# Kernel optimization log

Measured on AMD Instinct MI355X. Metric: run time of the kernel, lower is better.

The kernel has to match this reference:

```python
import jax, jax.numpy as jnp
import numpy as np

B, S, D = 2, 2048, 1024
H = 16
DK = D // H
SCALE = 1.0 / np.sqrt(DK)

def setup_inputs() -> dict:
    key = jax.random.key(0)
    ks = jax.random.split(key, 11)
    std = 1.0 / np.sqrt(D)
    return {
        "query": jax.random.normal(ks[0], (B, S, D), jnp.float32),
        "key":   jax.random.normal(ks[1], (B, S, D), jnp.float32),
        "value": jax.random.normal(ks[2], (B, S, D), jnp.float32),
        "Wq": jax.random.normal(ks[3], (D, H * DK), jnp.float32) * std,
        "bq": jnp.zeros((H * DK,), jnp.float32),
        "Wk": jax.random.normal(ks[4], (D, H * DK), jnp.float32) * std,
        "bk": jnp.zeros((H * DK,), jnp.float32),
        "Wv": jax.random.normal(ks[5], (D, H * DK), jnp.float32) * std,
        "bv": jnp.zeros((H * DK,), jnp.float32),
        "Wo": jax.random.normal(ks[6], (D, D), jnp.float32) * std,
        "bo": jnp.zeros((D,), jnp.float32),
    }

def reference(query, key, value, Wq, bq, Wk, bk, Wv, bv, Wo, bo):
    b, s, _ = query.shape
    # projections -> [b, s, h, d_k]
    q = (query @ Wq + bq).reshape(b, s, H, DK)
    k = (key   @ Wk + bk).reshape(b, s, H, DK)
    v = (value @ Wv + bv).reshape(b, s, H, DK)
    # scores [b, i, j, h]
    scores = jnp.einsum('bihd,bjhd->bijh', q, k) * SCALE
    attn = jax.nn.softmax(scores, axis=2)  # softmax over key dim j
    # dropout rate 0.0 (eval mode) -> identity
    x = jnp.einsum('bijh,bjhd->bihd', attn, v).reshape(b, s, H * DK)
    return x @ Wo + bo
```

## Files before the change

### kernel.cpp

```cpp
#include <hip/hip_runtime.h>
#include <hip/hip_bf16.h>
#include <math.h>
#include <stdint.h>

constexpr int Bb = 2, Ss = 2048, Dd = 1024, Hh = 16;
constexpr int Mm = Bb * Ss;
constexpr int Nn = Dd;
constexpr int Kk = Dd;
constexpr float QSCALE = 0.125f * 1.44269504088896340736f;

typedef unsigned short ushort_t;
typedef __attribute__((ext_vector_type(8))) short bf16x8;
typedef __attribute__((ext_vector_type(4))) float f32x4;

#if __has_builtin(__builtin_amdgcn_exp2f)
#define EXP2F(x) __builtin_amdgcn_exp2f(x)
#else
#define EXP2F(x) exp2f(x)
#endif

__device__ __forceinline__ ushort_t f2bf(float f) {
  union { float f; unsigned u; } v; v.f = f;
  return (ushort_t)((v.u + 0x7fff + ((v.u >> 16) & 1)) >> 16);
}

__device__ __forceinline__ void load16_lds(const void* g, void* l) {
  __builtin_amdgcn_global_load_lds(
      (const __attribute__((address_space(1))) void*)(uintptr_t)g,
      (__attribute__((address_space(3))) void*)(uint32_t)(uintptr_t)l, 16, 0, 0);
}

__global__ __launch_bounds__(256) void convert_qkv(
    const float* __restrict__ q, const float* __restrict__ k,
    const float* __restrict__ v, ushort_t* __restrict__ out) {
  const int z = blockIdx.z;
  const float* src = (z == 0) ? q : (z == 1) ? k : v;
  ushort_t* dst = out + (size_t)z * Mm * Kk;
  const size_t idx = ((size_t)blockIdx.x * 256 + threadIdx.x) * 4;
  const float4 val = *(const float4*)(src + idx);
  ushort4 o;
  o.x = f2bf(val.x); o.y = f2bf(val.y); o.z = f2bf(val.z); o.w = f2bf(val.w);
  *(ushort4*)(dst + idx) = o;
}

__global__ __launch_bounds__(256) void transpose_w(
    const float* __restrict__ Wq, const float* __restrict__ Wk,
    const float* __restrict__ Wv, const float* __restrict__ Wo,
    ushort_t* __restrict__ Wt) {
  const int z = blockIdx.z;
  const float* W = (z == 0) ? Wq : (z == 1) ? Wk : (z == 2) ? Wv : Wo;
  ushort_t* out = Wt + (size_t)z * Kk * Nn;
  __shared__ float t[64][65];
  const int tid = threadIdx.x;
  const int n0 = blockIdx.x * 64, k0 = blockIdx.y * 64;
  const int lr = tid >> 4, lc = (tid & 15) * 4;
#pragma unroll
  for (int i = 0; i < 4; i++) {
    const int r = lr + i * 16;
    const float4 v = *(const float4*)(W + (size_t)(k0 + r) * Nn + n0 + lc);
    t[r][lc] = v.x; t[r][lc + 1] = v.y; t[r][lc + 2] = v.z; t[r][lc + 3] = v.w;
  }
  __syncthreads();
  const int n = tid >> 2, kc = (tid & 3) * 16;
  ushort_t tmp[16];
#pragma unroll
  for (int j = 0; j < 16; j++) tmp[j] = f2bf(t[kc + j][n]);
  ushort_t* op = out + (size_t)(n0 + n) * Kk + k0 + kc;
  ((uint4*)op)[0] = ((uint4*)tmp)[0];
  ((uint4*)op)[1] = ((uint4*)tmp)[1];
}

template <int BN, bool OUT_BF16>
__global__ __launch_bounds__(256) void gemm_mfma(
    const ushort_t* __restrict__ Abase, size_t a_stride,
    const ushort_t* __restrict__ Wbase, size_t w_stride,
    const float* __restrict__ bias0, const float* __restrict__ bias1,
    const float* __restrict__ bias2, void* __restrict__ Cbase, size_t c_stride,
    float scale_z0, ushort_t* __restrict__ vt_out) {
  constexpr int BM = 128, BK = 32;
  constexpr int WM = (BN == 128) ? 64 : 32;
  constexpr int MT_ = WM / 16, NT_ = 4;
  __shared__ ushort_t As[BM * BK];
  __shared__ ushort_t Bs[BN * BK];
  const int tid = threadIdx.x, lane = tid & 63, wid = tid >> 6;
  const int z = blockIdx.z;
  const ushort_t* A = Abase + (size_t)z * a_stride;
  const ushort_t* Wt = Wbase + (size_t)z * w_stride;
  const float* bias = (z == 0) ? bias0 : (z == 1) ? bias1 : bias2;
  const float sc = (z == 0) ? scale_z0 : 1.0f;
  const int m0 = blockIdx.y * BM, n0 = blockIdx.x * BN;
  const int wm = (BN == 128) ? (wid >> 1) * 64 : wid * 32;
  const int wn = (BN == 128) ? (wid & 1) * 64 : 0;
  const int quad = lane >> 4, r16 = lane & 15;
  const int srow = lane >> 2;
  const int scol = (lane & 3) * 8;

  f32x4 acc[MT_][NT_];
#pragma unroll
  for (int m = 0; m < MT_; m++)
#pragma unroll
    for (int n = 0; n < NT_; n++) acc[m][n] = f32x4{0.f, 0.f, 0.f, 0.f};

  for (int k0 = 0; k0 < Kk; k0 += BK) {
    __syncthreads();
#pragma unroll
    for (int i = 0; i < BM / 64; i++) {
      const int I = wid * (BM / 64) + i;
      load16_lds(A + (size_t)(m0 + I * 16 + srow) * Kk + k0 + scol, As + I * 512);
    }
#pragma unroll
    for (int i = 0; i < BN / 64; i++) {
      const int I = wid * (BN / 64) + i;
      load16_lds(Wt + (size_t)(n0 + I * 16 + srow) * Kk + k0 + scol, Bs + I * 512);
    }
    __syncthreads();
    bf16x8 af[MT_], bfr[NT_];
#pragma unroll
    for (int m = 0; m < MT_; m++)
      af[m] = *(const bf16x8*)(As + (wm + m * 16 + r16) * BK + quad * 8);
#pragma unroll
    for (int n = 0; n < NT_; n++)
      bfr[n] = *(const bf16x8*)(Bs + (wn + n * 16 + r16) * BK + quad * 8);
#pragma unroll
    for (int m = 0; m < MT_; m++)
#pragma unroll
      for (int n = 0; n < NT_; n++)
        acc[m][n] =
            __builtin_amdgcn_mfma_f32_16x16x32_bf16(af[m], bfr[n], acc[m][n], 0, 0, 0);
  }

  if (vt_out != nullptr && z == 2) {
#pragma unroll
    for (int m = 0; m < MT_; m++) {
      const int gr0 = m0 + wm + m * 16 + quad * 4;
      const int bb = gr0 >> 11, s = gr0 & 2047;
#pragma unroll
      for (int n = 0; n < NT_; n++) {
        const int gc = n0 + wn + n * 16 + r16;
        const float bv = bias[gc];
        ushort4 o;
        o.x = f2bf(acc[m][n][0] + bv);
        o.y = f2bf(acc[m][n][1] + bv);
        o.z = f2bf(acc[m][n][2] + bv);
        o.w = f2bf(acc[m][n][3] + bv);
        *(ushort4*)(vt_out + ((size_t)bb * Dd + gc) * Ss + s) = o;
      }
    }
    return;
  }
#pragma unroll
  for (int m = 0; m < MT_; m++) {
#pragma unroll
    for (int n = 0; n < NT_; n++) {
      const int gc = n0 + wn + n * 16 + r16;
      const float bv = bias[gc];
#pragma unroll
      for (int r = 0; r < 4; r++) {
        const int gr = m0 + wm + m * 16 + quad * 4 + r;
        const float v = (acc[m][n][r] + bv) * sc;
        if (OUT_BF16)
          ((ushort_t*)Cbase)[(size_t)z * c_stride + (size_t)gr * Nn + gc] = f2bf(v);
        else
          ((float*)Cbase)[(size_t)z * c_stride + (size_t)gr * Nn + gc] = v;
      }
    }
  }
}

__global__ __launch_bounds__(256) void flash_mfma(
    const ushort_t* __restrict__ Qp, const ushort_t* __restrict__ Kp,
    const ushort_t* __restrict__ Vt, ushort_t* __restrict__ Xp) {
  __shared__ ushort_t Ks[64 * 64];
  __shared__ ushort_t Vts[64 * 64];
  __shared__ ushort_t Ps[64 * 72];
  const int tid = threadIdx.x, lane = tid & 63, wid = tid >> 6;
  const int qt = blockIdx.x, h = blockIdx.y, b = blockIdx.z;
  const int quad = lane >> 4, r16 = lane & 15;
  const int row8 = lane >> 3;
  const int colsw = ((lane & 7) ^ (row8 & 7)) * 8;
  const int swz = (r16 & 7);

  const int qrow = wid * 16 + r16;
  const ushort_t* Qg = Qp + ((size_t)(b * Ss + qt * 64)) * Dd + h * 64;
  const ushort_t* Kg = Kp + ((size_t)b * Ss) * Dd + h * 64;
  const ushort_t* Vg = Vt + ((size_t)b * Dd + h * 64) * Ss;

  bf16x8 qf[2];
#pragma unroll
  for (int ks = 0; ks < 2; ks++)
    qf[ks] = *(const bf16x8*)(Qg + (size_t)qrow * Dd + ks * 32 + quad * 8);

  f32x4 acc[4];
  float rs = 0.f;
#pragma unroll
  for (int mt = 0; mt < 4; mt++) acc[mt] = f32x4{0.f, 0.f, 0.f, 0.f};

  for (int kt = 0; kt < Ss / 64; kt++) {
    __syncthreads();
#pragma unroll
    for (int i = 0; i < 2; i++) {
      const int I = wid * 2 + i;
      load16_lds(Kg + (size_t)(kt * 64 + I * 8 + row8) * Dd + colsw, Ks + I * 512);
      load16_lds(Vg + (size_t)(I * 8 + row8) * Ss + kt * 64 + colsw, Vts + I * 512);
    }
    __syncthreads();

    f32x4 sacc[4];
#pragma unroll
    for (int mm = 0; mm < 4; mm++) sacc[mm] = f32x4{0.f, 0.f, 0.f, 0.f};
#pragma unroll
    for (int ks = 0; ks < 2; ks++) {
      bf16x8 kf[4];
#pragma unroll
      for (int mm = 0; mm < 4; mm++)
        kf[mm] = *(const bf16x8*)(
            Ks + (mm * 16 + r16) * 64 + (((ks * 4 + quad) ^ swz) * 8));
#pragma unroll
      for (int mm = 0; mm < 4; mm++)
        sacc[mm] = __builtin_amdgcn_mfma_f32_16x16x32_bf16(
            kf[mm], qf[ks], sacc[mm], 0, 0, 0);
    }

#pragma unroll
    for (int mm = 0; mm < 4; mm++) {
      float p0 = EXP2F(sacc[mm][0]), p1 = EXP2F(sacc[mm][1]);
      float p2 = EXP2F(sacc[mm][2]), p3 = EXP2F(sacc[mm][3]);
      rs += (p0 + p1) + (p2 + p3);
      union { __hip_bfloat162 h; unsigned u; } lo, hi;
      lo.h = __float22bfloat162_rn(make_float2(p0, p1));
      hi.h = __float22bfloat162_rn(make_float2(p2, p3));
      *(uint2*)(Ps + qrow * 72 + mm * 16 + quad * 4) = make_uint2(lo.u, hi.u);
    }

#pragma unroll
    for (int ks = 0; ks < 2; ks++) {
      bf16x8 vf[4];
#pragma unroll
      for (int mt = 0; mt < 4; mt++)
        vf[mt] = *(const bf16x8*)(
            Vts + (mt * 16 + r16) * 64 + (((ks * 4 + quad) ^ swz) * 8));
      const bf16x8 pf = *(const bf16x8*)(Ps + qrow * 72 + ks * 32 + quad * 8);
#pragma unroll
      for (int mt = 0; mt < 4; mt++)
        acc[mt] = __builtin_amdgcn_mfma_f32_16x16x32_bf16(
            vf[mt], pf, acc[mt], 0, 0, 0);
    }
  }

  rs += __shfl_xor(rs, 16, 64);
  rs += __shfl_xor(rs, 32, 64);
  const float inv = 1.0f / rs;

#pragma unroll
  for (int mt = 0; mt < 4; mt++) {
    ushort4 o;
    o.x = f2bf(acc[mt][0] * inv);
    o.y = f2bf(acc[mt][1] * inv);
    o.z = f2bf(acc[mt][2] * inv);
    o.w = f2bf(acc[mt][3] * inv);
    *(ushort4*)(Xp + (size_t)(b * Ss + qt * 64 + qrow) * Dd +
                h * 64 + mt * 16 + quad * 4) = o;
  }
}

extern "C" void kernel_launch(void* const* d_in, const int* in_sizes, int n_in,
                              void* d_out, int out_size, void* d_ws,
                              size_t ws_size, hipStream_t stream) {
  const float* q  = (const float*)d_in[0];
  const float* k  = (const float*)d_in[1];
  const float* v  = (const float*)d_in[2];
  const float* Wq = (const float*)d_in[3];
  const float* bq = (const float*)d_in[4];
  const float* Wk = (const float*)d_in[5];
  const float* bk = (const float*)d_in[6];
  const float* Wv = (const float*)d_in[7];
  const float* bv = (const float*)d_in[8];
  const float* Wo = (const float*)d_in[9];
  const float* bo = (const float*)d_in[10];

  ushort_t* ws = (ushort_t*)d_ws;
  const size_t MD = (size_t)Mm * Kk;
  const size_t KN = (size_t)Kk * Nn;
  ushort_t* qkvb = ws;
  ushort_t* Wt   = ws + 3 * MD;
  ushort_t* QKVp = Wt + 4 * KN;
  ushort_t* Vtp  = QKVp + 3 * MD;
  ushort_t* Xp   = qkvb;

  convert_qkv<<<dim3(4096, 1, 3), 256, 0, stream>>>(q, k, v, qkvb);
  transpose_w<<<dim3(16, 16, 4), 256, 0, stream>>>(Wq, Wk, Wv, Wo, Wt);
  gemm_mfma<128, true><<<dim3(Nn / 128, Mm / 128, 3), 256, 0, stream>>>(
      qkvb, MD, Wt, KN, bq, bk, bv, QKVp, MD, QSCALE, Vtp);
  flash_mfma<<<dim3(Ss / 64, Hh, Bb), 256, 0, stream>>>(QKVp, QKVp + MD, Vtp, Xp);
  gemm_mfma<64, false><<<dim3(Nn / 64, Mm / 128, 1), 256, 0, stream>>>(
      Xp, 0, Wt + 3 * KN, 0, bo, bo, bo, d_out, 0, 1.0f, nullptr);
}
```

Measured before the change: 248.8 us.

## Widen GEMM K-tile with swizzled LDS, double flash KV tile, separate V transpose

The GEMM K-step grows from 32 to 64 and uses an XOR-swizzled LDS layout to avoid bank conflicts, halving the number of barrier-separated iterations. The flash kernel now processes 128 keys per iteration in two 64-key halves, cutting sync overhead per key. The strided transposed V store in the GEMM epilogue is replaced by a separate transpose_v kernel, trading an extra launch and memory pass for coalesced writes. LDS use per block grows, which may reduce occupancy.

```diff
diff --git a/kernel.cpp b/kernel.cpp
--- a/kernel.cpp
+++ b/kernel.cpp
@@ -70,14 +70,37 @@
   ((uint4*)op)[1] = ((uint4*)tmp)[1];
 }
 
+__global__ __launch_bounds__(256) void transpose_v(
+    const ushort_t* __restrict__ Vp, ushort_t* __restrict__ Vt) {
+  __shared__ ushort_t t[64][68];
+  const int tid = threadIdx.x;
+  const int s0 = blockIdx.x * 64, h = blockIdx.y, b = blockIdx.z;
+  const int lr = tid >> 4, lc = (tid & 15) * 4;
+#pragma unroll
+  for (int i = 0; i < 4; i++) {
+    const int r = lr + i * 16;
+    const ushort4 v =
+        *(const ushort4*)(Vp + (size_t)(b * Ss + s0 + r) * Dd + h * 64 + lc);
+    *(ushort4*)&t[r][lc] = v;
+  }
+  __syncthreads();
+  const int d = tid >> 2, sc = (tid & 3) * 16;
+  ushort_t tmp[16];
+#pragma unroll
+  for (int j = 0; j < 16; j++) tmp[j] = t[sc + j][d];
+  ushort_t* op = Vt + ((size_t)b * Dd + h * 64 + d) * Ss + s0 + sc;
+  ((uint4*)op)[0] = ((uint4*)tmp)[0];
+  ((uint4*)op)[1] = ((uint4*)tmp)[1];
+}
+
 template <int BN, bool OUT_BF16>
 __global__ __launch_bounds__(256) void gemm_mfma(
     const ushort_t* __restrict__ Abase, size_t a_stride,
     const ushort_t* __restrict__ Wbase, size_t w_stride,
     const float* __restrict__ bias0, const float* __restrict__ bias1,
     const float* __restrict__ bias2, void* __restrict__ Cbase, size_t c_stride,
-    float scale_z0, ushort_t* __restrict__ vt_out) {
-  constexpr int BM = 128, BK = 32;
+    float scale_z0) {
+  constexpr int BM = 128, BK = 64;
   constexpr int WM = (BN == 128) ? 64 : 32;
   constexpr int MT_ = WM / 16, NT_ = 4;
   __shared__ ushort_t As[BM * BK];
@@ -92,8 +115,9 @@
   const int wm = (BN == 128) ? (wid >> 1) * 64 : wid * 32;
   const int wn = (BN == 128) ? (wid & 1) * 64 : 0;
   const int quad = lane >> 4, r16 = lane & 15;
-  const int srow = lane >> 2;
-  const int scol = (lane & 3) * 8;
+  const int row8 = lane >> 3;
+  const int colsw = ((lane & 7) ^ (row8 & 7)) * 8;
+  const int swz = r16 & 7;
 
   f32x4 acc[MT_][NT_];
 #pragma unroll
@@ -104,50 +128,35 @@
   for (int k0 = 0; k0 < Kk; k0 += BK) {
     __syncthreads();
 #pragma unroll
-    for (int i = 0; i < BM / 64; i++) {
-      const int I = wid * (BM / 64) + i;
-      load16_lds(A + (size_t)(m0 + I * 16 + srow) * Kk + k0 + scol, As + I * 512);
-    }
-#pragma unroll
-    for (int i = 0; i < BN / 64; i++) {
-      const int I = wid * (BN / 64) + i;
-      load16_lds(Wt + (size_t)(n0 + I * 16 + srow) * Kk + k0 + scol, Bs + I * 512);
+    for (int i = 0; i < BM / 32; i++) {
+      const int I = wid * (BM / 32) + i;
+      load16_lds(A + (size_t)(m0 + I * 8 + row8) * Kk + k0 + colsw, As + I * 512);
+    }
+#pragma unroll
+    for (int i = 0; i < BN / 32; i++) {
+      const int I = wid * (BN / 32) + i;
+      load16_lds(Wt + (size_t)(n0 + I * 8 + row8) * Kk + k0 + colsw, Bs + I * 512);
     }
     __syncthreads();
-    bf16x8 af[MT_], bfr[NT_];
-#pragma unroll
-    for (int m = 0; m < MT_; m++)
-      af[m] = *(const bf16x8*)(As + (wm + m * 16 + r16) * BK + quad * 8);
-#pragma unroll
-    for (int n = 0; n < NT_; n++)
-      bfr[n] = *(const bf16x8*)(Bs + (wn + n * 16 + r16) * BK + quad * 8);
-#pragma unroll
-    for (int m = 0; m < MT_; m++)
+#pragma unroll
+    for (int ks = 0; ks < 2; ks++) {
+      const int ko = ((ks * 4 + quad) ^ swz) * 8;
+      bf16x8 af[MT_], bfr[NT_];
+#pragma unroll
+      for (int m = 0; m < MT_; m++)
+        af[m] = *(const bf16x8*)(As + (wm + m * 16 + r16) * BK + ko);
 #pragma unroll
       for (int n = 0; n < NT_; n++)
-        acc[m][n] =
-            __builtin_amdgcn_mfma_f32_16x16x32_bf16(af[m], bfr[n], acc[m][n], 0, 0, 0);
-  }
-
-  if (vt_out != nullptr && z == 2) {
-#pragma unroll
-    for (int m = 0; m < MT_; m++) {
-      const int gr0 = m0 + wm + m * 16 + quad * 4;
-      const int bb = gr0 >> 11, s = gr0 & 2047;
-#pragma unroll
-      for (int n = 0; n < NT_; n++) {
-        const int gc = n0 + wn + n * 16 + r16;
-        const float bv = bias[gc];
-        ushort4 o;
-        o.x = f2bf(acc[m][n][0] + bv);
-        o.y = f2bf(acc[m][n][1] + bv);
-        o.z = f2bf(acc[m][n][2] + bv);
-        o.w = f2bf(acc[m][n][3] + bv);
-        *(ushort4*)(vt_out + ((size_t)bb * Dd + gc) * Ss + s) = o;
-      }
-    }
-    return;
-  }
+        bfr[n] = *(const bf16x8*)(Bs + (wn + n * 16 + r16) * BK + ko);
+#pragma unroll
+      for (int m = 0; m < MT_; m++)
+#pragma unroll
+        for (int n = 0; n < NT_; n++)
+          acc[m][n] = __builtin_amdgcn_mfma_f32_16x16x32_bf16(
+              af[m], bfr[n], acc[m][n], 0, 0, 0);
+    }
+  }
+
 #pragma unroll
   for (int m = 0; m < MT_; m++) {
 #pragma unroll
@@ -170,15 +179,15 @@
 __global__ __launch_bounds__(256) void flash_mfma(
     const ushort_t* __restrict__ Qp, const ushort_t* __restrict__ Kp,
     const ushort_t* __restrict__ Vt, ushort_t* __restrict__ Xp) {
-  __shared__ ushort_t Ks[64 * 64];
-  __shared__ ushort_t Vts[64 * 64];
-  __shared__ ushort_t Ps[64 * 72];
+  __shared__ ushort_t Ks[128 * 64];
+  __shared__ ushort_t Vts[2 * 64 * 64];
+  __shared__ ushort_t Ps[2][64 * 72];
   const int tid = threadIdx.x, lane = tid & 63, wid = tid >> 6;
   const int qt = blockIdx.x, h = blockIdx.y, b = blockIdx.z;
   const int quad = lane >> 4, r16 = lane & 15;
   const int row8 = lane >> 3;
   const int colsw = ((lane & 7) ^ (row8 & 7)) * 8;
-  const int swz = (r16 & 7);
+  const int swz = r16 & 7;
 
   const int qrow = wid * 16 + r16;
   const ushort_t* Qg = Qp + ((size_t)(b * Ss + qt * 64)) * Dd + h * 64;
@@ -195,55 +204,76 @@
 #pragma unroll
   for (int mt = 0; mt < 4; mt++) acc[mt] = f32x4{0.f, 0.f, 0.f, 0.f};
 
-  for (int kt = 0; kt < Ss / 64; kt++) {
+  for (int kt = 0; kt < Ss / 128; kt++) {
     __syncthreads();
 #pragma unroll
-    for (int i = 0; i < 2; i++) {
-      const int I = wid * 2 + i;
-      load16_lds(Kg + (size_t)(kt * 64 + I * 8 + row8) * Dd + colsw, Ks + I * 512);
-      load16_lds(Vg + (size_t)(I * 8 + row8) * Ss + kt * 64 + colsw, Vts + I * 512);
+    for (int i = 0; i < 4; i++) {
+      const int I = wid * 4 + i;
+      load16_lds(Kg + (size_t)(kt * 128 + I * 8 + row8) * Dd + colsw,
+                 Ks + I * 512);
+    }
+#pragma unroll
+    for (int i = 0; i < 4; i++) {
+      const int I = wid * 4 + i;
+      const int hf = I >> 3, rr = (I & 7) * 8;
+      load16_lds(Vg + (size_t)(rr + row8) * Ss + kt * 128 + hf * 64 + colsw,
+                 Vts + I * 512);
     }
     __syncthreads();
 
-    f32x4 sacc[4];
-#pragma unroll
-    for (int mm = 0; mm < 4; mm++) sacc[mm] = f32x4{0.f, 0.f, 0.f, 0.f};
-#pragma unroll
-    for (int ks = 0; ks < 2; ks++) {
-      bf16x8 kf[4];
-#pragma unroll
-      for (int mm = 0; mm < 4; mm++)
-        kf[mm] = *(const bf16x8*)(
-            Ks + (mm * 16 + r16) * 64 + (((ks * 4 + quad) ^ swz) * 8));
-#pragma unroll
-      for (int mm = 0; mm < 4; mm++)
-        sacc[mm] = __builtin_amdgcn_mfma_f32_16x16x32_bf16(
-            kf[mm], qf[ks], sacc[mm], 0, 0, 0);
-    }
-
-#pragma unroll
-    for (int mm = 0; mm < 4; mm++) {
-      float p0 = EXP2F(sacc[mm][0]), p1 = EXP2F(sacc[mm][1]);
-      float p2 = EXP2F(sacc[mm][2]), p3 = EXP2F(sacc[mm][3]);
-      rs += (p0 + p1) + (p2 + p3);
-      union { __hip_bfloat162 h; unsigned u; } lo, hi;
-      lo.h = __float22bfloat162_rn(make_float2(p0, p1));
-      hi.h = __float22bfloat162_rn(make_float2(p2, p3));
-      *(uint2*)(Ps + qrow * 72 + mm * 16 + quad * 4) = make_uint2(lo.u, hi.u);
-    }
-
-#pragma unroll
-    for (int ks = 0; ks < 2; ks++) {
-      bf16x8 vf[4];
-#pragma unroll
-      for (int mt = 0; mt < 4; mt++)
-        vf[mt] = *(const bf16x8*)(
-            Vts + (mt * 16 + r16) * 64 + (((ks * 4 + quad) ^ swz) * 8));
-      const bf16x8 pf = *(const bf16x8*)(Ps + qrow * 72 + ks * 32 + quad * 8);
-#pragma unroll
-      for (int mt = 0; mt < 4; mt++)
-        acc[mt] = __builtin_amdgcn_mfma_f32_16x16x32_bf16(
-            vf[mt], pf, acc[mt], 0, 0, 0);
+    f32x4 sacc[2][4];
+#pragma unroll
+    for (int hf = 0; hf < 2; hf++)
+#pragma unroll
+      for (int mm = 0; mm < 4; mm++) sacc[hf][mm] = f32x4{0.f, 0.f, 0.f, 0.f};
+#pragma unroll
+    for (int hf = 0; hf < 2; hf++) {
+#pragma unroll
+      for (int ks = 0; ks < 2; ks++) {
+        const int ko = ((ks * 4 + quad) ^ swz) * 8;
+        bf16x8 kf[4];
+#pragma unroll
+        for (int mm = 0; mm < 4; mm++)
+          kf[mm] = *(const bf16x8*)(Ks + (hf * 64 + mm * 16 + r16) * 64 + ko);
+#pragma unroll
+        for (int mm = 0; mm < 4; mm++)
+          sacc[hf][mm] = __builtin_amdgcn_mfma_f32_16x16x32_bf16(
+              kf[mm], qf[ks], sacc[hf][mm], 0, 0, 0);
+      }
+    }
+
+#pragma unroll
+    for (int hf = 0; hf < 2; hf++) {
+#pragma unroll
+      for (int mm = 0; mm < 4; mm++) {
+        float p0 = EXP2F(sacc[hf][mm][0]), p1 = EXP2F(sacc[hf][mm][1]);
+        float p2 = EXP2F(sacc[hf][mm][2]), p3 = EXP2F(sacc[hf][mm][3]);
+        rs += (p0 + p1) + (p2 + p3);
+        union { __hip_bfloat162 hh; unsigned u; } lo, hi;
+        lo.hh = __float22bfloat162_rn(make_float2(p0, p1));
+        hi.hh = __float22bfloat162_rn(make_float2(p2, p3));
+        *(uint2*)(Ps[hf] + qrow * 72 + mm * 16 + quad * 4) =
+            make_uint2(lo.u, hi.u);
+      }
+    }
+
+#pragma unroll
+    for (int hf = 0; hf < 2; hf++) {
+#pragma unroll
+      for (int ks = 0; ks < 2; ks++) {
+        const int ko = ((ks * 4 + quad) ^ swz) * 8;
+        bf16x8 vf[4];
+#pragma unroll
+        for (int mt = 0; mt < 4; mt++)
+          vf[mt] = *(const bf16x8*)(
+              Vts + hf * 4096 + (mt * 16 + r16) * 64 + ko);
+        const bf16x8 pf =
+            *(const bf16x8*)(Ps[hf] + qrow * 72 + ks * 32 + quad * 8);
+#pragma unroll
+        for (int mt = 0; mt < 4; mt++)
+          acc[mt] = __builtin_amdgcn_mfma_f32_16x16x32_bf16(
+              vf[mt], pf, acc[mt], 0, 0, 0);
+      }
     }
   }
 
@@ -290,8 +320,9 @@
   convert_qkv<<<dim3(4096, 1, 3), 256, 0, stream>>>(q, k, v, qkvb);
   transpose_w<<<dim3(16, 16, 4), 256, 0, stream>>>(Wq, Wk, Wv, Wo, Wt);
   gemm_mfma<128, true><<<dim3(Nn / 128, Mm / 128, 3), 256, 0, stream>>>(
-      qkvb, MD, Wt, KN, bq, bk, bv, QKVp, MD, QSCALE, Vtp);
+      qkvb, MD, Wt, KN, bq, bk, bv, QKVp, MD, QSCALE);
+  transpose_v<<<dim3(Ss / 64, Hh, Bb), 256, 0, stream>>>(QKVp + 2 * MD, Vtp);
   flash_mfma<<<dim3(Ss / 64, Hh, Bb), 256, 0, stream>>>(QKVp, QKVp + MD, Vtp, Xp);
   gemm_mfma<64, false><<<dim3(Nn / 64, Mm / 128, 1), 256, 0, stream>>>(
-      Xp, 0, Wt + 3 * KN, 0, bo, bo, bo, d_out, 0, 1.0f, nullptr);
-}
+      Xp, 0, Wt + 3 * KN, 0, bo, bo, bo, d_out, 0, 1.0f);
+}
```

Measured after the change: 250.4 us. About the same (+0.6%).

## Switch GEMMs to 32x32x16 MFMA and move V transpose to separate kernel

Applied to the files above, without the earlier changes.

The projection GEMMs now use 32x32x16 bf16 MFMA tiles instead of 16x16x32, so each wave issues fewer, larger matrix instructions and loads fewer fragments from LDS per step. The fused V-transposed store in the GEMM epilogue is removed. A separate transpose_v kernel now builds Vt from the projected V, which costs an extra launch and an extra read and write of V. The flash kernel only gets cosmetic hoisting of the swizzle offset.

```diff
diff --git a/kernel.cpp b/kernel.cpp
--- a/kernel.cpp
+++ b/kernel.cpp
@@ -12,6 +12,7 @@
 typedef unsigned short ushort_t;
 typedef __attribute__((ext_vector_type(8))) short bf16x8;
 typedef __attribute__((ext_vector_type(4))) float f32x4;
+typedef __attribute__((ext_vector_type(16))) float f32x16;
 
 #if __has_builtin(__builtin_amdgcn_exp2f)
 #define EXP2F(x) __builtin_amdgcn_exp2f(x)
@@ -70,16 +71,40 @@
   ((uint4*)op)[1] = ((uint4*)tmp)[1];
 }
 
+__global__ __launch_bounds__(256) void transpose_v(
+    const ushort_t* __restrict__ Vp, ushort_t* __restrict__ Vt) {
+  __shared__ ushort_t t[64][68];
+  const int tid = threadIdx.x;
+  const int s0 = blockIdx.x * 64, h = blockIdx.y, b = blockIdx.z;
+  const int lr = tid >> 4, lc = (tid & 15) * 4;
+#pragma unroll
+  for (int i = 0; i < 4; i++) {
+    const int r = lr + i * 16;
+    const ushort4 v =
+        *(const ushort4*)(Vp + (size_t)(b * Ss + s0 + r) * Dd + h * 64 + lc);
+    *(ushort4*)&t[r][lc] = v;
+  }
+  __syncthreads();
+  const int d = tid >> 2, sc = (tid & 3) * 16;
+  ushort_t tmp[16];
+#pragma unroll
+  for (int j = 0; j < 16; j++) tmp[j] = t[sc + j][d];
+  ushort_t* op = Vt + ((size_t)b * Dd + h * 64 + d) * Ss + s0 + sc;
+  ((uint4*)op)[0] = ((uint4*)tmp)[0];
+  ((uint4*)op)[1] = ((uint4*)tmp)[1];
+}
+
 template <int BN, bool OUT_BF16>
 __global__ __launch_bounds__(256) void gemm_mfma(
     const ushort_t* __restrict__ Abase, size_t a_stride,
     const ushort_t* __restrict__ Wbase, size_t w_stride,
     const float* __restrict__ bias0, const float* __restrict__ bias1,
     const float* __restrict__ bias2, void* __restrict__ Cbase, size_t c_stride,
-    float scale_z0, ushort_t* __restrict__ vt_out) {
+    float scale_z0) {
   constexpr int BM = 128, BK = 32;
   constexpr int WM = (BN == 128) ? 64 : 32;
-  constexpr int MT_ = WM / 16, NT_ = 4;
+  constexpr int MT_ = WM / 32;
+  constexpr int NT_ = 2;
   __shared__ ushort_t As[BM * BK];
   __shared__ ushort_t Bs[BN * BK];
   const int tid = threadIdx.x, lane = tid & 63, wid = tid >> 6;
@@ -91,15 +116,17 @@
   const int m0 = blockIdx.y * BM, n0 = blockIdx.x * BN;
   const int wm = (BN == 128) ? (wid >> 1) * 64 : wid * 32;
   const int wn = (BN == 128) ? (wid & 1) * 64 : 0;
-  const int quad = lane >> 4, r16 = lane & 15;
+  const int r32 = lane & 31, half = lane >> 5;
   const int srow = lane >> 2;
   const int scol = (lane & 3) * 8;
 
-  f32x4 acc[MT_][NT_];
+  f32x16 acc[MT_][NT_];
 #pragma unroll
   for (int m = 0; m < MT_; m++)
 #pragma unroll
-    for (int n = 0; n < NT_; n++) acc[m][n] = f32x4{0.f, 0.f, 0.f, 0.f};
+    for (int n = 0; n < NT_; n++)
+#pragma unroll
+      for (int i = 0; i < 16; i++) acc[m][n][i] = 0.f;
 
   for (int k0 = 0; k0 < Kk; k0 += BK) {
     __syncthreads();
@@ -114,54 +141,46 @@
       load16_lds(Wt + (size_t)(n0 + I * 16 + srow) * Kk + k0 + scol, Bs + I * 512);
     }
     __syncthreads();
-    bf16x8 af[MT_], bfr[NT_];
+    bf16x8 af[MT_][2], bfr[NT_][2];
 #pragma unroll
     for (int m = 0; m < MT_; m++)
-      af[m] = *(const bf16x8*)(As + (wm + m * 16 + r16) * BK + quad * 8);
+#pragma unroll
+      for (int kin = 0; kin < 2; kin++)
+        af[m][kin] = *(const bf16x8*)(
+            As + (wm + m * 32 + r32) * BK + kin * 16 + half * 8);
 #pragma unroll
     for (int n = 0; n < NT_; n++)
-      bfr[n] = *(const bf16x8*)(Bs + (wn + n * 16 + r16) * BK + quad * 8);
-#pragma unroll
-    for (int m = 0; m < MT_; m++)
-#pragma unroll
-      for (int n = 0; n < NT_; n++)
-        acc[m][n] =
-            __builtin_amdgcn_mfma_f32_16x16x32_bf16(af[m], bfr[n], acc[m][n], 0, 0, 0);
-  }
-
-  if (vt_out != nullptr && z == 2) {
-#pragma unroll
-    for (int m = 0; m < MT_; m++) {
-      const int gr0 = m0 + wm + m * 16 + quad * 4;
-      const int bb = gr0 >> 11, s = gr0 & 2047;
-#pragma unroll
-      for (int n = 0; n < NT_; n++) {
-        const int gc = n0 + wn + n * 16 + r16;
-        const float bv = bias[gc];
-        ushort4 o;
-        o.x = f2bf(acc[m][n][0] + bv);
-        o.y = f2bf(acc[m][n][1] + bv);
-        o.z = f2bf(acc[m][n][2] + bv);
-        o.w = f2bf(acc[m][n][3] + bv);
-        *(ushort4*)(vt_out + ((size_t)bb * Dd + gc) * Ss + s) = o;
-      }
-    }
-    return;
-  }
+#pragma unroll
+      for (int kin = 0; kin < 2; kin++)
+        bfr[n][kin] = *(const bf16x8*)(
+            Bs + (wn + n * 32 + r32) * BK + kin * 16 + half * 8);
+#pragma unroll
+    for (int kin = 0; kin < 2; kin++)
+#pragma unroll
+      for (int m = 0; m < MT_; m++)
+#pragma unroll
+        for (int n = 0; n < NT_; n++)
+          acc[m][n] = __builtin_amdgcn_mfma_f32_32x32x16_bf16(
+              af[m][kin], bfr[n][kin], acc[m][n], 0, 0, 0);
+  }
+
 #pragma unroll
   for (int m = 0; m < MT_; m++) {
 #pragma unroll
     for (int n = 0; n < NT_; n++) {
-      const int gc = n0 + wn + n * 16 + r16;
+      const int gc = n0 + wn + n * 32 + r32;
       const float bv = bias[gc];
 #pragma unroll
-      for (int r = 0; r < 4; r++) {
-        const int gr = m0 + wm + m * 16 + quad * 4 + r;
-        const float v = (acc[m][n][r] + bv) * sc;
-        if (OUT_BF16)
-          ((ushort_t*)Cbase)[(size_t)z * c_stride + (size_t)gr * Nn + gc] = f2bf(v);
-        else
-          ((float*)Cbase)[(size_t)z * c_stride + (size_t)gr * Nn + gc] = v;
+      for (int g = 0; g < 4; g++) {
+#pragma unroll
+        for (int r = 0; r < 4; r++) {
+          const int gr = m0 + wm + m * 32 + r + 4 * half + 8 * g;
+          const float v = (acc[m][n][g * 4 + r] + bv) * sc;
+          if (OUT_BF16)
+            ((ushort_t*)Cbase)[(size_t)z * c_stride + (size_t)gr * Nn + gc] = f2bf(v);
+          else
+            ((float*)Cbase)[(size_t)z * c_stride + (size_t)gr * Nn + gc] = v;
+        }
       }
     }
   }
@@ -178,7 +197,7 @@
   const int quad = lane >> 4, r16 = lane & 15;
   const int row8 = lane >> 3;
   const int colsw = ((lane & 7) ^ (row8 & 7)) * 8;
-  const int swz = (r16 & 7);
+  const int swz = r16 & 7;
 
   const int qrow = wid * 16 + r16;
   const ushort_t* Qg = Qp + ((size_t)(b * Ss + qt * 64)) * Dd + h * 64;
@@ -210,11 +229,11 @@
     for (int mm = 0; mm < 4; mm++) sacc[mm] = f32x4{0.f, 0.f, 0.f, 0.f};
 #pragma unroll
     for (int ks = 0; ks < 2; ks++) {
+      const int ko = ((ks * 4 + quad) ^ swz) * 8;
       bf16x8 kf[4];
 #pragma unroll
       for (int mm = 0; mm < 4; mm++)
-        kf[mm] = *(const bf16x8*)(
-            Ks + (mm * 16 + r16) * 64 + (((ks * 4 + quad) ^ swz) * 8));
+        kf[mm] = *(const bf16x8*)(Ks + (mm * 16 + r16) * 64 + ko);
 #pragma unroll
       for (int mm = 0; mm < 4; mm++)
         sacc[mm] = __builtin_amdgcn_mfma_f32_16x16x32_bf16(
@@ -226,19 +245,19 @@
       float p0 = EXP2F(sacc[mm][0]), p1 = EXP2F(sacc[mm][1]);
       float p2 = EXP2F(sacc[mm][2]), p3 = EXP2F(sacc[mm][3]);
       rs += (p0 + p1) + (p2 + p3);
-      union { __hip_bfloat162 h; unsigned u; } lo, hi;
-      lo.h = __float22bfloat162_rn(make_float2(p0, p1));
-      hi.h = __float22bfloat162_rn(make_float2(p2, p3));
+      union { __hip_bfloat162 hh; unsigned u; } lo, hi;
+      lo.hh = __float22bfloat162_rn(make_float2(p0, p1));
+      hi.hh = __float22bfloat162_rn(make_float2(p2, p3));
       *(uint2*)(Ps + qrow * 72 + mm * 16 + quad * 4) = make_uint2(lo.u, hi.u);
     }
 
 #pragma unroll
     for (int ks = 0; ks < 2; ks++) {
+      const int ko = ((ks * 4 + quad) ^ swz) * 8;
       bf16x8 vf[4];
 #pragma unroll
       for (int mt = 0; mt < 4; mt++)
-        vf[mt] = *(const bf16x8*)(
-            Vts + (mt * 16 + r16) * 64 + (((ks * 4 + quad) ^ swz) * 8));
+        vf[mt] = *(const bf16x8*)(Vts + (mt * 16 + r16) * 64 + ko);
       const bf16x8 pf = *(const bf16x8*)(Ps + qrow * 72 + ks * 32 + quad * 8);
 #pragma unroll
       for (int mt = 0; mt < 4; mt++)
@@ -290,8 +309,9 @@
   convert_qkv<<<dim3(4096, 1, 3), 256, 0, stream>>>(q, k, v, qkvb);
   transpose_w<<<dim3(16, 16, 4), 256, 0, stream>>>(Wq, Wk, Wv, Wo, Wt);
   gemm_mfma<128, true><<<dim3(Nn / 128, Mm / 128, 3), 256, 0, stream>>>(
-      qkvb, MD, Wt, KN, bq, bk, bv, QKVp, MD, QSCALE, Vtp);
+      qkvb, MD, Wt, KN, bq, bk, bv, QKVp, MD, QSCALE);
+  transpose_v<<<dim3(Ss / 64, Hh, Bb), 256, 0, stream>>>(QKVp + 2 * MD, Vtp);
   flash_mfma<<<dim3(Ss / 64, Hh, Bb), 256, 0, stream>>>(QKVp, QKVp + MD, Vtp, Xp);
   gemm_mfma<64, false><<<dim3(Nn / 64, Mm / 128, 1), 256, 0, stream>>>(
-      Xp, 0, Wt + 3 * KN, 0, bo, bo, bo, d_out, 0, 1.0f, nullptr);
-}
+      Xp, 0, Wt + 3 * KN, 0, bo, bo, bo, d_out, 0, 1.0f);
+}
```

Measured after the change: 243.6 us. 1.02x faster.
